# Performance work log

Measured on AMD Instinct MI355X. Metric: run time of the kernel, lower is better.

The kernel has to match this reference:

```python
import jax, jax.numpy as jnp
import numpy as np

B, S, D = 4, 4096, 64

def setup_inputs() -> dict:
    key = jax.random.key(0)
    k1, k2, k3 = jax.random.split(key, 3)
    inputs = jax.random.normal(k1, (B, S, D), dtype=jnp.float32)
    rotation = jax.random.normal(k2, (D, D), dtype=jnp.float32)
    entangle = jax.random.normal(k3, (D, D), dtype=jnp.float32)
    return {"inputs": inputs, "rotation": rotation, "entangle": entangle}

def reference(inputs, rotation, entangle):
    # query/key projections: [B,S,D] @ [D,D] -> [B,S,D]
    query = jnp.einsum('bsd,de->bse', inputs, rotation)
    key = jnp.einsum('bsd,de->bse', inputs, entangle)
    scale = 1.0 / jnp.sqrt(jnp.float32(inputs.shape[-1]))
    # scores: [B,S,S] softmax over last axis
    scores = jax.nn.softmax(jnp.einsum('bqd,bkd->bqk', query, key) * scale, axis=-1)
    # values are the raw inputs (no value projection)
    return jnp.einsum('bqk,bkd->bqd', scores, inputs)
```

## Files before the change

kernel.cpp:

```cpp
#include <hip/hip_runtime.h>
#include <hip/hip_fp16.h>

#define BB 4
#define SS 4096
#define DD 64
#define NSPLIT 4
#define KT_PER (SS / 64 / NSPLIT)

typedef _Float16 half8 __attribute__((ext_vector_type(8)));
typedef _Float16 half4 __attribute__((ext_vector_type(4)));
typedef float floatx4 __attribute__((ext_vector_type(4)));

__global__ __launch_bounds__(256) void proj_kernel(
    const float* __restrict__ X, const float* __restrict__ R, const float* __restrict__ E,
    _Float16* __restrict__ Qhi, _Float16* __restrict__ Qlo,
    _Float16* __restrict__ Khi, _Float16* __restrict__ Klo,
    _Float16* __restrict__ Vt)
{
    __shared__ float Rs[64][64];
    __shared__ float Es[64][64];
    __shared__ float Xs[16][68];
    int t = threadIdx.x;
    long rowbase = (long)blockIdx.x * 16;

    for (int j = 0; j < 4; ++j) {
        int idx = j * 256 + t;
        int r = idx >> 4;
        int c = (idx & 15) * 4;
        *(float4*)&Rs[r][c] = ((const float4*)R)[idx];
        *(float4*)&Es[r][c] = ((const float4*)E)[idx];
    }
    *(float4*)&Xs[t >> 4][(t & 15) * 4] = ((const float4*)(X + rowbase * 64))[t];
    __syncthreads();

    int row = t >> 4;
    int c0 = (t & 15) * 4;
    float q[4] = {0.f, 0.f, 0.f, 0.f}, k[4] = {0.f, 0.f, 0.f, 0.f};
    for (int d = 0; d < 64; ++d) {
        float x = Xs[row][d];
        for (int j = 0; j < 4; ++j) {
            q[j] = fmaf(x, Rs[d][c0 + j], q[j]);
            k[j] = fmaf(x, Es[d][c0 + j], k[j]);
        }
    }
    long gq = (rowbase + row) * 64 + c0;
    half4 qh, ql, kh, kl;
    for (int j = 0; j < 4; ++j) {
        _Float16 h = (_Float16)q[j];
        qh[j] = h; ql[j] = (_Float16)(q[j] - (float)h);
        h = (_Float16)k[j];
        kh[j] = h; kl[j] = (_Float16)(k[j] - (float)h);
    }
    *(half4*)(Qhi + gq) = qh; *(half4*)(Qlo + gq) = ql;
    *(half4*)(Khi + gq) = kh; *(half4*)(Klo + gq) = kl;

    int d = t >> 2;
    int si = (t & 3) * 4;
    int b = (int)(rowbase >> 12);
    int sbase = (int)(rowbase & 4095);
    half4 v;
    for (int j = 0; j < 4; ++j) v[j] = (_Float16)Xs[si + j][d];
    *(half4*)(Vt + ((long)(b * 64 + d)) * SS + sbase + si) = v;
}

#define L2E 1.44269504088896340736f
#define PD 72

__global__ __launch_bounds__(256) void attn_partial(
    const _Float16* __restrict__ Qhi, const _Float16* __restrict__ Qlo,
    const _Float16* __restrict__ Khi, const _Float16* __restrict__ Klo,
    const _Float16* __restrict__ Vt,
    float* __restrict__ Op, float* __restrict__ Mp, float* __restrict__ Lp)
{
    __shared__ _Float16 Ksh[64][PD];
    __shared__ _Float16 Ksl[64][PD];
    __shared__ _Float16 Vs[64][PD];
    __shared__ _Float16 Ps[4][16][PD];

    int t = threadIdx.x;
    int wave = t >> 6;
    int lane = t & 63;
    int l15 = lane & 15;
    int quad = lane >> 4;
    int split = blockIdx.y;
    int b = blockIdx.z;
    int q0 = blockIdx.x * 64 + wave * 16;

    long qrow = ((long)b * SS + q0 + l15) * DD;
    half8 qa0h = *(const half8*)(Qhi + qrow + quad * 8);
    half8 qa1h = *(const half8*)(Qhi + qrow + 32 + quad * 8);
    half8 qa0l = *(const half8*)(Qlo + qrow + quad * 8);
    half8 qa1l = *(const half8*)(Qlo + qrow + 32 + quad * 8);

    floatx4 o[4];
    for (int i = 0; i < 4; ++i) o[i] = (floatx4){0.f, 0.f, 0.f, 0.f};
    float m_r[4] = {-1e30f, -1e30f, -1e30f, -1e30f};
    float l_r[4] = {0.f, 0.f, 0.f, 0.f};

    const float scale = 0.125f * L2E;

    for (int kt = split * KT_PER; kt < (split + 1) * KT_PER; ++kt) {
        {
            int rr = t >> 2;
            int cc = (t & 3) * 16;
            long koff = ((long)b * SS + kt * 64 + rr) * DD + cc;
            const uint4* khsrc = (const uint4*)(Khi + koff);
            uint4* khdst = (uint4*)&Ksh[rr][cc];
            khdst[0] = khsrc[0]; khdst[1] = khsrc[1];
            const uint4* klsrc = (const uint4*)(Klo + koff);
            uint4* kldst = (uint4*)&Ksl[rr][cc];
            kldst[0] = klsrc[0]; kldst[1] = klsrc[1];
            const uint4* vsrc = (const uint4*)(Vt + ((long)b * 64 + rr) * SS + kt * 64 + cc);
            uint4* vdst = (uint4*)&Vs[rr][cc];
            vdst[0] = vsrc[0]; vdst[1] = vsrc[1];
        }
        __syncthreads();

        floatx4 s[4];
        for (int ct = 0; ct < 4; ++ct) {
            floatx4 acc = {0.f, 0.f, 0.f, 0.f};
            half8 kb0h = *(const half8*)&Ksh[ct * 16 + l15][quad * 8];
            half8 kb1h = *(const half8*)&Ksh[ct * 16 + l15][32 + quad * 8];
            half8 kb0l = *(const half8*)&Ksl[ct * 16 + l15][quad * 8];
            half8 kb1l = *(const half8*)&Ksl[ct * 16 + l15][32 + quad * 8];
            acc = __builtin_amdgcn_mfma_f32_16x16x32_f16(qa0h, kb0h, acc, 0, 0, 0);
            acc = __builtin_amdgcn_mfma_f32_16x16x32_f16(qa1h, kb1h, acc, 0, 0, 0);
            acc = __builtin_amdgcn_mfma_f32_16x16x32_f16(qa0h, kb0l, acc, 0, 0, 0);
            acc = __builtin_amdgcn_mfma_f32_16x16x32_f16(qa1h, kb1l, acc, 0, 0, 0);
            acc = __builtin_amdgcn_mfma_f32_16x16x32_f16(qa0l, kb0h, acc, 0, 0, 0);
            acc = __builtin_amdgcn_mfma_f32_16x16x32_f16(qa1l, kb1h, acc, 0, 0, 0);
            s[ct] = acc;
        }

        float p[4][4];
        for (int r = 0; r < 4; ++r) {
            float mt = fmaxf(fmaxf(s[0][r], s[1][r]), fmaxf(s[2][r], s[3][r]));
            for (int off = 8; off; off >>= 1)
                mt = fmaxf(mt, __shfl_xor(mt, off));
            mt *= scale;
            float mn = fmaxf(m_r[r], mt);
            float alpha = exp2f(m_r[r] - mn);
            m_r[r] = mn;
            float rs = 0.f;
            for (int ct = 0; ct < 4; ++ct) {
                float pv = exp2f(s[ct][r] * scale - mn);
                p[ct][r] = pv;
                rs += pv;
            }
            for (int off = 8; off; off >>= 1)
                rs += __shfl_xor(rs, off);
            l_r[r] = l_r[r] * alpha + rs;
            for (int dt = 0; dt < 4; ++dt) o[dt][r] *= alpha;
        }

        for (int ct = 0; ct < 4; ++ct)
            for (int r = 0; r < 4; ++r)
                Ps[wave][quad * 4 + r][ct * 16 + l15] = (_Float16)p[ct][r];

        for (int h = 0; h < 2; ++h) {
            half8 pa = *(const half8*)&Ps[wave][l15][h * 32 + quad * 8];
            for (int dt = 0; dt < 4; ++dt) {
                half8 vb = *(const half8*)&Vs[dt * 16 + l15][h * 32 + quad * 8];
                o[dt] = __builtin_amdgcn_mfma_f32_16x16x32_f16(pa, vb, o[dt], 0, 0, 0);
            }
        }
        __syncthreads();
    }

    long pbase = ((long)b * NSPLIT + split) * SS;
    for (int r = 0; r < 4; ++r) {
        int q = q0 + quad * 4 + r;
        long orow = (pbase + q) * DD;
        for (int dt = 0; dt < 4; ++dt)
            Op[orow + dt * 16 + l15] = o[dt][r];
        if (l15 == 0) {
            Mp[pbase + q] = m_r[r];
            Lp[pbase + q] = l_r[r];
        }
    }
}

__global__ __launch_bounds__(256) void combine_kernel(
    const float* __restrict__ Op, const float* __restrict__ Mp,
    const float* __restrict__ Lp, float* __restrict__ Out)
{
    int t = threadIdx.x;
    int qi = t >> 4;
    int d4 = (t & 15) * 4;
    long gq = (long)blockIdx.x * 16 + qi;
    int b = (int)(gq >> 12);
    int s = (int)(gq & 4095);

    float m = -1e30f;
    for (int i = 0; i < NSPLIT; ++i)
        m = fmaxf(m, Mp[((long)b * NSPLIT + i) * SS + s]);
    float l = 0.f;
    float4 o = {0.f, 0.f, 0.f, 0.f};
    for (int i = 0; i < NSPLIT; ++i) {
        long pb = ((long)b * NSPLIT + i) * SS + s;
        float a = exp2f(Mp[pb] - m);
        l = fmaf(Lp[pb], a, l);
        float4 oi = *(const float4*)(Op + pb * DD + d4);
        o.x = fmaf(oi.x, a, o.x); o.y = fmaf(oi.y, a, o.y);
        o.z = fmaf(oi.z, a, o.z); o.w = fmaf(oi.w, a, o.w);
    }
    float inv = 1.f / l;
    float4 r = {o.x * inv, o.y * inv, o.z * inv, o.w * inv};
    *(float4*)(Out + gq * DD + d4) = r;
}

extern "C" void kernel_launch(void* const* d_in, const int* in_sizes, int n_in,
                              void* d_out, int out_size, void* d_ws, size_t ws_size,
                              hipStream_t stream) {
    const float* X = (const float*)d_in[0];
    const float* R = (const float*)d_in[1];
    const float* E = (const float*)d_in[2];
    float* Out = (float*)d_out;

    const size_t N = (size_t)BB * SS * DD;
    _Float16* Qhi = (_Float16*)d_ws;
    _Float16* Qlo = Qhi + N;
    _Float16* Khi = Qlo + N;
    _Float16* Klo = Khi + N;
    _Float16* Vt  = Klo + N;
    float* Op = (float*)(Vt + N);
    float* Mp = Op + (size_t)BB * NSPLIT * SS * DD;
    float* Lp = Mp + (size_t)BB * NSPLIT * SS;

    proj_kernel<<<dim3(BB * SS / 16), 256, 0, stream>>>(X, R, E, Qhi, Qlo, Khi, Klo, Vt);
    attn_partial<<<dim3(SS / 64, NSPLIT, BB), 256, 0, stream>>>(Qhi, Qlo, Khi, Klo, Vt, Op, Mp, Lp);
    combine_kernel<<<dim3(BB * SS / 16), 256, 0, stream>>>(Op, Mp, Lp, Out);
}
```

Before: 148.3 us.

## Prefetch K/V tiles into registers and transpose score MFMA for per-lane softmax

The attention kernel now loads the next K/V tile into registers while the current tile is computed, which hides global load latency behind the MFMA work. The QK^T MFMA operands are swapped so that each lane holds scores for a single query row. Row max and sum then need only two cross-quad shuffles, and the probabilities are packed to fp16 with cvt_pkrtz. The rescale factor is redistributed with __shfl, occupancy is hinted with launch_bounds(256,4), and the projection kernel uses float4 LDS reads with unrolling. The costs are higher register pressure and round-toward-zero rounding of P.

```diff
diff --git a/kernel.cpp b/kernel.cpp
--- a/kernel.cpp
+++ b/kernel.cpp
@@ -9,6 +9,7 @@
 
 typedef _Float16 half8 __attribute__((ext_vector_type(8)));
 typedef _Float16 half4 __attribute__((ext_vector_type(4)));
+typedef __fp16 fp16x2 __attribute__((ext_vector_type(2)));
 typedef float floatx4 __attribute__((ext_vector_type(4)));
 
 __global__ __launch_bounds__(256) void proj_kernel(
@@ -36,12 +37,15 @@
     int row = t >> 4;
     int c0 = (t & 15) * 4;
     float q[4] = {0.f, 0.f, 0.f, 0.f}, k[4] = {0.f, 0.f, 0.f, 0.f};
+#pragma unroll 4
     for (int d = 0; d < 64; ++d) {
         float x = Xs[row][d];
-        for (int j = 0; j < 4; ++j) {
-            q[j] = fmaf(x, Rs[d][c0 + j], q[j]);
-            k[j] = fmaf(x, Es[d][c0 + j], k[j]);
-        }
+        float4 rv = *(const float4*)&Rs[d][c0];
+        float4 ev = *(const float4*)&Es[d][c0];
+        q[0] = fmaf(x, rv.x, q[0]); q[1] = fmaf(x, rv.y, q[1]);
+        q[2] = fmaf(x, rv.z, q[2]); q[3] = fmaf(x, rv.w, q[3]);
+        k[0] = fmaf(x, ev.x, k[0]); k[1] = fmaf(x, ev.y, k[1]);
+        k[2] = fmaf(x, ev.z, k[2]); k[3] = fmaf(x, ev.w, k[3]);
     }
     long gq = (rowbase + row) * 64 + c0;
     half4 qh, ql, kh, kl;
@@ -66,7 +70,7 @@
 #define L2E 1.44269504088896340736f
 #define PD 72
 
-__global__ __launch_bounds__(256) void attn_partial(
+__global__ __launch_bounds__(256, 4) void attn_partial(
     const _Float16* __restrict__ Qhi, const _Float16* __restrict__ Qlo,
     const _Float16* __restrict__ Khi, const _Float16* __restrict__ Klo,
     const _Float16* __restrict__ Vt,
@@ -94,68 +98,97 @@
 
     floatx4 o[4];
     for (int i = 0; i < 4; ++i) o[i] = (floatx4){0.f, 0.f, 0.f, 0.f};
-    float m_r[4] = {-1e30f, -1e30f, -1e30f, -1e30f};
-    float l_r[4] = {0.f, 0.f, 0.f, 0.f};
+    float m_q = -1e30f;
+    float l_q = 0.f;
 
     const float scale = 0.125f * L2E;
 
-    for (int kt = split * KT_PER; kt < (split + 1) * KT_PER; ++kt) {
+    int rr = t >> 2;
+    int cc = (t & 3) * 16;
+    long kbase = ((long)b * SS + rr) * DD + cc;
+    long vbase = ((long)b * 64 + rr) * SS + cc;
+
+    int kt = split * KT_PER;
+    uint4 rh0, rh1, rl0, rl1, rv0, rv1;
+    {
+        const uint4* khsrc = (const uint4*)(Khi + kbase + (long)kt * 64 * DD);
+        rh0 = khsrc[0]; rh1 = khsrc[1];
+        const uint4* klsrc = (const uint4*)(Klo + kbase + (long)kt * 64 * DD);
+        rl0 = klsrc[0]; rl1 = klsrc[1];
+        const uint4* vsrc = (const uint4*)(Vt + vbase + kt * 64);
+        rv0 = vsrc[0]; rv1 = vsrc[1];
+    }
+
+    for (int i = 0; i < KT_PER; ++i) {
+        if (i > 0) __syncthreads();
         {
-            int rr = t >> 2;
-            int cc = (t & 3) * 16;
-            long koff = ((long)b * SS + kt * 64 + rr) * DD + cc;
-            const uint4* khsrc = (const uint4*)(Khi + koff);
             uint4* khdst = (uint4*)&Ksh[rr][cc];
-            khdst[0] = khsrc[0]; khdst[1] = khsrc[1];
-            const uint4* klsrc = (const uint4*)(Klo + koff);
+            khdst[0] = rh0; khdst[1] = rh1;
             uint4* kldst = (uint4*)&Ksl[rr][cc];
-            kldst[0] = klsrc[0]; kldst[1] = klsrc[1];
-            const uint4* vsrc = (const uint4*)(Vt + ((long)b * 64 + rr) * SS + kt * 64 + cc);
+            kldst[0] = rl0; kldst[1] = rl1;
             uint4* vdst = (uint4*)&Vs[rr][cc];
-            vdst[0] = vsrc[0]; vdst[1] = vsrc[1];
+            vdst[0] = rv0; vdst[1] = rv1;
         }
         __syncthreads();
+
+        int ktn = (i + 1 < KT_PER) ? (kt + 1) : kt;
+        {
+            const uint4* khsrc = (const uint4*)(Khi + kbase + (long)ktn * 64 * DD);
+            rh0 = khsrc[0]; rh1 = khsrc[1];
+            const uint4* klsrc = (const uint4*)(Klo + kbase + (long)ktn * 64 * DD);
+            rl0 = klsrc[0]; rl1 = klsrc[1];
+            const uint4* vsrc = (const uint4*)(Vt + vbase + ktn * 64);
+            rv0 = vsrc[0]; rv1 = vsrc[1];
+        }
+        kt = ktn;
 
         floatx4 s[4];
         for (int ct = 0; ct < 4; ++ct) {
             floatx4 acc = {0.f, 0.f, 0.f, 0.f};
-            half8 kb0h = *(const half8*)&Ksh[ct * 16 + l15][quad * 8];
-            half8 kb1h = *(const half8*)&Ksh[ct * 16 + l15][32 + quad * 8];
-            half8 kb0l = *(const half8*)&Ksl[ct * 16 + l15][quad * 8];
-            half8 kb1l = *(const half8*)&Ksl[ct * 16 + l15][32 + quad * 8];
-            acc = __builtin_amdgcn_mfma_f32_16x16x32_f16(qa0h, kb0h, acc, 0, 0, 0);
-            acc = __builtin_amdgcn_mfma_f32_16x16x32_f16(qa1h, kb1h, acc, 0, 0, 0);
-            acc = __builtin_amdgcn_mfma_f32_16x16x32_f16(qa0h, kb0l, acc, 0, 0, 0);
-            acc = __builtin_amdgcn_mfma_f32_16x16x32_f16(qa1h, kb1l, acc, 0, 0, 0);
-            acc = __builtin_amdgcn_mfma_f32_16x16x32_f16(qa0l, kb0h, acc, 0, 0, 0);
-            acc = __builtin_amdgcn_mfma_f32_16x16x32_f16(qa1l, kb1h, acc, 0, 0, 0);
+            half8 ka0h = *(const half8*)&Ksh[ct * 16 + l15][quad * 8];
+            half8 ka1h = *(const half8*)&Ksh[ct * 16 + l15][32 + quad * 8];
+            half8 ka0l = *(const half8*)&Ksl[ct * 16 + l15][quad * 8];
+            half8 ka1l = *(const half8*)&Ksl[ct * 16 + l15][32 + quad * 8];
+            acc = __builtin_amdgcn_mfma_f32_16x16x32_f16(ka0h, qa0h, acc, 0, 0, 0);
+            acc = __builtin_amdgcn_mfma_f32_16x16x32_f16(ka1h, qa1h, acc, 0, 0, 0);
+            acc = __builtin_amdgcn_mfma_f32_16x16x32_f16(ka0h, qa0l, acc, 0, 0, 0);
+            acc = __builtin_amdgcn_mfma_f32_16x16x32_f16(ka1h, qa1l, acc, 0, 0, 0);
+            acc = __builtin_amdgcn_mfma_f32_16x16x32_f16(ka0l, qa0h, acc, 0, 0, 0);
+            acc = __builtin_amdgcn_mfma_f32_16x16x32_f16(ka1l, qa1h, acc, 0, 0, 0);
             s[ct] = acc;
         }
 
-        float p[4][4];
-        for (int r = 0; r < 4; ++r) {
-            float mt = fmaxf(fmaxf(s[0][r], s[1][r]), fmaxf(s[2][r], s[3][r]));
-            for (int off = 8; off; off >>= 1)
-                mt = fmaxf(mt, __shfl_xor(mt, off));
-            mt *= scale;
-            float mn = fmaxf(m_r[r], mt);
-            float alpha = exp2f(m_r[r] - mn);
-            m_r[r] = mn;
-            float rs = 0.f;
-            for (int ct = 0; ct < 4; ++ct) {
-                float pv = exp2f(s[ct][r] * scale - mn);
-                p[ct][r] = pv;
-                rs += pv;
-            }
-            for (int off = 8; off; off >>= 1)
-                rs += __shfl_xor(rs, off);
-            l_r[r] = l_r[r] * alpha + rs;
-            for (int dt = 0; dt < 4; ++dt) o[dt][r] *= alpha;
-        }
-
+        float mt = s[0][0];
         for (int ct = 0; ct < 4; ++ct)
             for (int r = 0; r < 4; ++r)
-                Ps[wave][quad * 4 + r][ct * 16 + l15] = (_Float16)p[ct][r];
+                mt = fmaxf(mt, s[ct][r]);
+        mt = fmaxf(mt, __shfl_xor(mt, 16));
+        mt = fmaxf(mt, __shfl_xor(mt, 32));
+        mt *= scale;
+        float mn = fmaxf(m_q, mt);
+        float alpha = exp2f(m_q - mn);
+        m_q = mn;
+
+        float rs = 0.f;
+        for (int ct = 0; ct < 4; ++ct) {
+            float p0 = exp2f(s[ct][0] * scale - mn);
+            float p1 = exp2f(s[ct][1] * scale - mn);
+            float p2 = exp2f(s[ct][2] * scale - mn);
+            float p3 = exp2f(s[ct][3] * scale - mn);
+            rs += (p0 + p1) + (p2 + p3);
+            union { fp16x2 h2[2]; half4 h4; } u;
+            u.h2[0] = __builtin_amdgcn_cvt_pkrtz(p0, p1);
+            u.h2[1] = __builtin_amdgcn_cvt_pkrtz(p2, p3);
+            *(half4*)&Ps[wave][l15][ct * 16 + quad * 4] = u.h4;
+        }
+        rs += __shfl_xor(rs, 16);
+        rs += __shfl_xor(rs, 32);
+        l_q = l_q * alpha + rs;
+
+        for (int r = 0; r < 4; ++r) {
+            float a = __shfl(alpha, quad * 4 + r);
+            o[0][r] *= a; o[1][r] *= a; o[2][r] *= a; o[3][r] *= a;
+        }
 
         for (int h = 0; h < 2; ++h) {
             half8 pa = *(const half8*)&Ps[wave][l15][h * 32 + quad * 8];
@@ -164,7 +197,6 @@
                 o[dt] = __builtin_amdgcn_mfma_f32_16x16x32_f16(pa, vb, o[dt], 0, 0, 0);
             }
         }
-        __syncthreads();
     }
 
     long pbase = ((long)b * NSPLIT + split) * SS;
@@ -173,10 +205,10 @@
         long orow = (pbase + q) * DD;
         for (int dt = 0; dt < 4; ++dt)
             Op[orow + dt * 16 + l15] = o[dt][r];
-        if (l15 == 0) {
-            Mp[pbase + q] = m_r[r];
-            Lp[pbase + q] = l_r[r];
-        }
+    }
+    if (quad == 0) {
+        Mp[pbase + q0 + l15] = m_q;
+        Lp[pbase + q0 + l15] = l_q;
     }
 }
 
```

Result: faster. 119.8 us (-19.2%).
